# Kernel tuning notes

Measured on AMD Instinct MI355X. Metric: run time of the kernel, lower is better.

The kernel has to match this reference:

```python
import jax, jax.numpy as jnp
import numpy as np

B, S, D = 2, 4096, 768
H, W = 12, 128          # W = one-sided attention window; S % (2*W) == 0
DFF = 3072
HD = D // H
EPS = 1e-6


def band_attention(q, k, v, w):
    """Sliding-window (banded) attention, sliding_chunks-equivalent.
    q,k,v: (B, S, H, HD); q pre-scaled by 1/sqrt(HD).
    Returns context (B, S, D) and band probs (B, H, S, 2w+1)."""
    b, s, h, hd = q.shape
    n = s // w                                    # number of query blocks
    qb = q.reshape(b, n, w, h, hd)
    kp = jnp.pad(k, ((0, 0), (w, w), (0, 0), (0, 0)))   # zero-pad seq by w each side
    vp = jnp.pad(v, ((0, 0), (w, w), (0, 0), (0, 0)))
    # block i needs padded keys [i*w, i*w + 3w)  (blocks i-1, i, i+1)
    gidx = jnp.arange(n)[:, None] * w + jnp.arange(3 * w)[None, :]   # (n, 3w)
    kb = kp[:, gidx]                              # (b, n, 3w, h, hd)
    vb = vp[:, gidx]
    scores = jnp.einsum('bnthd,bnjhd->bhntj', qb, kb)   # (b,h,n,w,3w)
    t = jnp.arange(w)[:, None]                    # (w,1) pos within block
    j = jnp.arange(3 * w)[None, :]                # (1,3w)
    rel = j - w - t                               # relative key offset, valid in [-w,w]
    pos = jnp.arange(n)[:, None, None] * w + (j - w)     # (n,1,3w) global key pos
    valid = (jnp.abs(rel) <= w)[None] & (pos >= 0) & (pos < s)  # (n,w,3w)
    scores = jnp.where(valid[None, None], scores, -jnp.inf)
    probs = jax.nn.softmax(scores, axis=-1)
    out = jnp.einsum('bhntj,bnjhd->bnthd', probs, vb).reshape(b, s, h * hd)
    # extract the (2w+1) diagonals: offset d -> column j = t + d
    jj = jnp.arange(w)[:, None] + jnp.arange(2 * w + 1)[None, :]     # (w, 2w+1)
    attw = jnp.take_along_axis(probs, jj[None, None, None], axis=-1)
    return out, attw.reshape(b, h, s, 2 * w + 1)


def setup_inputs() -> dict:
    key = jax.random.key(0)
    ks = jax.random.split(key, 12)
    def lin(k, fan_in, shape):
        return (jax.random.normal(k, shape, jnp.float32) / np.sqrt(fan_in)).astype(jnp.float32)
    return {
        'src': jax.random.normal(ks[0], (B, S, D), jnp.float32),
        'Wq': lin(ks[1], D, (D, D)), 'bq': jnp.zeros((D,), jnp.float32),
        'Wk': lin(ks[2], D, (D, D)), 'bk': jnp.zeros((D,), jnp.float32),
        'Wv': lin(ks[3], D, (D, D)), 'bv': jnp.zeros((D,), jnp.float32),
        'W1': lin(ks[4], D, (D, DFF)), 'b1': jnp.zeros((DFF,), jnp.float32),
        'W2': lin(ks[5], DFF, (DFF, D)), 'b2': jnp.zeros((D,), jnp.float32),
        'g2': 1.0 + 0.1 * jax.random.normal(ks[6], (D,), jnp.float32),
        'beta2': 0.1 * jax.random.normal(ks[7], (D,), jnp.float32),
    }


def reference(src, Wq, bq, Wk, bk, Wv, bv, W1, b1, W2, b2, g2, beta2):
    b, s, d = src.shape
    # self-attention (allenai LongformerSelfAttention: q/k/v linears, no out proj)
    q = ((src @ Wq + bq) / np.sqrt(HD).astype(np.float32)).reshape(b, s, H, HD)
    k = (src @ Wk + bk).reshape(b, s, H, HD)
    v = (src @ Wv + bv).reshape(b, s, H, HD)
    attn_out, attn_w = band_attention(q, k, v, W)
    x = src + attn_out                      # residual (dropout=0, eval)
    # PositionalwiseFeedForward: Linear -> ReLU -> Linear
    ffn = jnp.maximum(x @ W1 + b1, 0.0) @ W2 + b2
    y = x + ffn
    # post-norm (normalize_before=False: only norm2 is applied)
    mu = jnp.mean(y, axis=-1, keepdims=True)
    var = jnp.mean(jnp.square(y - mu), axis=-1, keepdims=True)
    out = g2 * (y - mu) / jnp.sqrt(var + EPS) + beta2
    return out, attn_w
```

## Files before the change

kernel.cpp:

```cpp
#include <hip/hip_runtime.h>
#include <hip/hip_bf16.h>
#include <stdint.h>

#define NB 2
#define NS 4096
#define ND 768
#define NH 12
#define NW 128
#define NDFF 3072
#define NHD 64
#define NCH 32

typedef __attribute__((ext_vector_type(8))) short bf16x8;
typedef __attribute__((ext_vector_type(4))) short s16x4;
typedef __attribute__((ext_vector_type(4))) float f32x4;
typedef __attribute__((ext_vector_type(4))) int i32x4;

__device__ __forceinline__ float bf2f(short u) {
    union { unsigned int i; float f; } c;
    c.i = ((unsigned int)(unsigned short)u) << 16;
    return c.f;
}
__device__ __forceinline__ short f2bf(float f) {
    union { float f; unsigned int i; } c;
    c.f = f;
    unsigned int x = c.i;
    return (short)((x + 0x7fffu + ((x >> 16) & 1u)) >> 16);
}
__device__ __forceinline__ unsigned int cvtpk(float lo, float hi) {
    unsigned int r;
    asm("v_cvt_pk_bf16_f32 %0, %1, %2" : "=v"(r) : "v"(lo), "v"(hi));
    return r;
}
__device__ __forceinline__ float ubits_lo(unsigned u) {
    union { unsigned i; float f; } c; c.i = u << 16; return c.f;
}
__device__ __forceinline__ float ubits_hi(unsigned u) {
    union { unsigned i; float f; } c; c.i = u & 0xffff0000u; return c.f;
}

__device__ __forceinline__ void gl16(const void* g, const void* l) {
    __builtin_amdgcn_global_load_lds(
        (const __attribute__((address_space(1))) void*)g,
        (__attribute__((address_space(3))) void*)l, 16, 0, 0);
}

__global__ __launch_bounds__(256) void cast_bf16(const float* __restrict__ in,
                                                 short* __restrict__ out, int n4) {
    int i = blockIdx.x * 256 + threadIdx.x;
    if (i < n4) {
        f32x4 v = ((const f32x4*)in)[i];
        s16x4 o;
        o[0] = f2bf(v[0]); o[1] = f2bf(v[1]); o[2] = f2bf(v[2]); o[3] = f2bf(v[3]);
        ((s16x4*)out)[i] = o;
    }
}

__global__ __launch_bounds__(256) void transpose_cast(const float* __restrict__ in,
                                                      short* __restrict__ out,
                                                      int K, int N) {
    __shared__ float tile[32][33];
    int kb = blockIdx.y * 32, nb = blockIdx.x * 32;
    int tx = threadIdx.x & 31, ty = threadIdx.x >> 5;
    #pragma unroll
    for (int r = ty; r < 32; r += 8)
        tile[r][tx] = in[(long)(kb + r) * N + nb + tx];
    __syncthreads();
    #pragma unroll
    for (int r = ty; r < 32; r += 8)
        out[(long)(nb + r) * K + kb + tx] = f2bf(tile[tx][r]);
}

template<int MODE>
__global__ __launch_bounds__(256, 2) void gemmdb(
    const short* __restrict__ A,
    const short* __restrict__ Bt,
    const float* __restrict__ b0,
    const float* __restrict__ b1,
    const float* __restrict__ b2,
    void* __restrict__ outp,
    const short* __restrict__ xres,
    int M, int N, int K, int gx)
{
    __shared__ short lds[2][256 * 64];
    const int KT = K >> 6;

    int cpx = gridDim.x >> 3;
    int bid = blockIdx.x;
    int tile = (bid & 7) * cpx + (bid >> 3);
    int n0 = (tile % gx) * 128;
    int m0 = (tile / gx) * 128;

    int tid = threadIdx.x;
    int wid = tid >> 6, lane = tid & 63;
    int wr = wid >> 1, wc = wid & 1;
    int g = lane >> 4, lr = lane & 15;

    int rl = lane >> 3, sl = lane & 7;
    int soff = (sl ^ rl) << 3;
    const short* gA[4];
    const short* gB[4];
    #pragma unroll
    for (int c = 0; c < 4; ++c) {
        int row = c * 32 + wid * 8 + rl;
        gA[c] = A + (long)(m0 + row) * K + soff;
        gB[c] = Bt + (long)(n0 + row) * K + soff;
    }

    f32x4 acc[4][4];
    #pragma unroll
    for (int a = 0; a < 4; ++a)
        #pragma unroll
        for (int c = 0; c < 4; ++c)
            acc[a][c] = (f32x4){0.f, 0.f, 0.f, 0.f};

    auto stage = [&](int t, int buf) {
        long ko = (long)t << 6;
        #pragma unroll
        for (int c = 0; c < 4; ++c) {
            int lbase = (c * 32 + wid * 8) * 64;
            gl16(gA[c] + ko, &lds[buf][lbase]);
            gl16(gB[c] + ko, &lds[buf][128 * 64 + lbase]);
        }
    };

    stage(0, 0);
    asm volatile("s_waitcnt vmcnt(0)" ::: "memory");
    __builtin_amdgcn_s_barrier();

    int buf = 0;
    for (int t = 0; t < KT; ++t) {
        if (t + 1 < KT) stage(t + 1, buf ^ 1);
        const short* bufA = lds[buf];
        const short* bufB = lds[buf] + 128 * 64;
        bf16x8 af[2][4], bfr[2][4];
        #pragma unroll
        for (int kk = 0; kk < 2; ++kk) {
            int ph = (((kk << 2) + g) ^ (lr & 7)) << 3;
            #pragma unroll
            for (int mt = 0; mt < 4; ++mt)
                af[kk][mt] = *(const bf16x8*)&bufA[(wr * 64 + mt * 16 + lr) * 64 + ph];
            #pragma unroll
            for (int nt = 0; nt < 4; ++nt)
                bfr[kk][nt] = *(const bf16x8*)&bufB[(wc * 64 + nt * 16 + lr) * 64 + ph];
        }
        #pragma unroll
        for (int kk = 0; kk < 2; ++kk)
            #pragma unroll
            for (int mt = 0; mt < 4; ++mt)
                #pragma unroll
                for (int nt = 0; nt < 4; ++nt)
                    acc[mt][nt] = __builtin_amdgcn_mfma_f32_16x16x32_bf16(
                        af[kk][mt], bfr[kk][nt], acc[mt][nt], 0, 0, 0);
        asm volatile("s_waitcnt vmcnt(0)" ::: "memory");
        __builtin_amdgcn_s_barrier();
        buf ^= 1;
    }

    int mr0 = m0 + wr * 64;
    int nc0 = n0 + wc * 64;
    if (MODE == 4) {
        int proj = n0 / 768;
        const float* bp = (proj == 0) ? b0 : (proj == 1) ? b1 : b2;
        float scl = (proj == 0) ? 0.125f : 1.0f;
        short* obase = (short*)outp + (long)proj * ((long)NB * NS * ND);
        #pragma unroll
        for (int mt = 0; mt < 4; ++mt) {
            #pragma unroll
            for (int nt = 0; nt < 4; ++nt) {
                int c = nc0 + nt * 16 + lr - proj * 768;
                int hh = c >> 6, hd = c & 63;
                float bv = bp[c];
                if (proj == 2) {
                    int m = mr0 + mt * 16 + (g << 2);
                    int bbi = m >> 12, s = m & (NS - 1);
                    s16x4 ov;
                    ov[0] = f2bf(acc[mt][nt][0] + bv);
                    ov[1] = f2bf(acc[mt][nt][1] + bv);
                    ov[2] = f2bf(acc[mt][nt][2] + bv);
                    ov[3] = f2bf(acc[mt][nt][3] + bv);
                    *(s16x4*)&obase[((long)(bbi * NH + hh) * NHD + hd) * NS + s] = ov;
                } else {
                    #pragma unroll
                    for (int i = 0; i < 4; ++i) {
                        int m = mr0 + mt * 16 + (g << 2) + i;
                        int bbi = m >> 12, s = m & (NS - 1);
                        obase[((long)(bbi * NH + hh) * NS + s) * NHD + hd] =
                            f2bf((acc[mt][nt][i] + bv) * scl);
                    }
                }
            }
        }
    } else {
        #pragma unroll
        for (int mt = 0; mt < 4; ++mt) {
            #pragma unroll
            for (int nt = 0; nt < 4; ++nt) {
                int col = nc0 + nt * 16 + lr;
                float bv = b0[col];
                #pragma unroll
                for (int i = 0; i < 4; ++i) {
                    int m = mr0 + mt * 16 + (g << 2) + i;
                    float v = acc[mt][nt][i];
                    if (MODE == 2) {
                        v = fmaxf(v + bv, 0.f);
                        ((short*)outp)[(long)m * NDFF + col] = f2bf(v);
                    } else {
                        v = v + bv + bf2f(xres[(long)m * ND + col]);
                        ((float*)outp)[(long)m * ND + col] = v;
                    }
                }
            }
        }
    }
}

__global__ __launch_bounds__(512, 2) void attn_kernel(
    const short* __restrict__ qg,
    const short* __restrict__ kg,
    const short* __restrict__ vtg,
    const float* __restrict__ src,
    float* __restrict__ attw,
    short* __restrict__ xb)
{
    __shared__ short kvs[384 * 64];

    int blk = blockIdx.x;
    int ch = blk & 31;
    int tmp = blk >> 5;
    int h = tmp % NH;
    int b = tmp / NH;
    int tid = threadIdx.x;
    int wid = tid >> 6;
    int lane = tid & 63;
    int g = lane >> 4, lr = lane & 15;
    long bh = (long)(b * NH + h);
    long kbase = bh * NS * NHD;
    int srow0 = ch * NW;
    int t0 = wid << 4;
    int tl = t0 + lr;

    {
        int rsub = lane >> 3;
        int pc = lane & 7;
        int lc = pc ^ rsub;
        #pragma unroll
        for (int i = 0; i < 6; ++i) {
            int inst = wid * 6 + i;
            int j = inst * 8 + rsub;
            int s = srow0 - NW + j;
            s = s < 0 ? 0 : (s >= NS ? NS - 1 : s);
            gl16(&kg[kbase + (long)s * NHD + lc * 8], &kvs[inst * 512 + lane * 8]);
        }
    }
    bf16x8 aq[2];
    #pragma unroll
    for (int kk = 0; kk < 2; ++kk)
        aq[kk] = *(const bf16x8*)&qg[kbase + (long)(srow0 + tl) * NHD + (kk << 5) + (g << 3)];

    asm volatile("s_waitcnt vmcnt(0)" ::: "memory");
    __builtin_amdgcn_s_barrier();
    __builtin_amdgcn_sched_barrier(0);

    unsigned pku0[12][2], pku1[12][2];
    float m0, s0, m1, s1;
    auto half_pass = [&](int jtb, unsigned (&pk)[12][2], float& mh, float& sh) {
        f32x4 sc[12];
        #pragma unroll
        for (int q = 0; q < 12; ++q) {
            int jt = jtb + q;
            f32x4 a = (f32x4){0.f, 0.f, 0.f, 0.f};
            #pragma unroll
            for (int kk = 0; kk < 2; ++kk) {
                int phys = (((kk << 2) + g) ^ (lr & 7)) << 3;
                bf16x8 bk = *(const bf16x8*)&kvs[(jt * 16 + lr) * 64 + phys];
                a = __builtin_amdgcn_mfma_f32_16x16x32_bf16(bk, aq[kk], a, 0, 0, 0);
            }
            sc[q] = a;
        }
        float mx = -3.0e30f;
        #pragma unroll
        for (int q = 0; q < 12; ++q) {
            int j0 = (jtb + q) * 16 + (g << 2);
            #pragma unroll
            for (int i = 0; i < 4; ++i) {
                int j = j0 + i;
                int sp = srow0 - NW + j;
                bool ok = (sp >= 0) && (sp < NS) && (j >= tl) && (j <= tl + 2 * NW);
                float v = ok ? sc[q][i] : -3.0e30f;
                sc[q][i] = v;
                mx = fmaxf(mx, v);
            }
        }
        mx = fmaxf(mx, __shfl_xor(mx, 16, 64));
        mx = fmaxf(mx, __shfl_xor(mx, 32, 64));
        float sm = 0.f;
        #pragma unroll
        for (int q = 0; q < 12; ++q) {
            #pragma unroll
            for (int i = 0; i < 4; ++i) {
                float v = sc[q][i];
                float p = (v > -1.0e30f) ? __expf(v - mx) : 0.0f;
                sc[q][i] = p;
                sm += p;
            }
            pk[q][0] = cvtpk(sc[q][0], sc[q][1]);
            pk[q][1] = cvtpk(sc[q][2], sc[q][3]);
        }
        sm += __shfl_xor(sm, 16, 64);
        sm += __shfl_xor(sm, 32, 64);
        mh = mx; sh = sm;
    };

    auto stageV = [&](int hf) {
        #pragma unroll
        for (int i = 0; i < 3; ++i) {
            int v = wid * 3 + i;
            int fc = hf * 1536 + v * 64 + lane;
            int hd = fc / 48;
            int pc = fc % 48;
            int lc = (pc & ~7) | ((pc & 7) ^ (hd & 7));
            int scol = srow0 - NW + lc * 8;
            scol = scol < 0 ? 0 : (scol > NS - 8 ? NS - 8 : scol);
            gl16(&vtg[(bh * NHD + hd) * NS + scol],
                 &kvs[hf * 12288 + v * 512 + lane * 8]);
        }
    };

    half_pass(0, pku0, m0, s0);
    asm volatile("s_waitcnt lgkmcnt(0)" ::: "memory");
    __builtin_amdgcn_s_barrier();
    __builtin_amdgcn_sched_barrier(0);
    stageV(0);

    half_pass(12, pku1, m1, s1);
    asm volatile("s_waitcnt lgkmcnt(0)" ::: "memory");
    __builtin_amdgcn_s_barrier();
    __builtin_amdgcn_sched_barrier(0);
    stageV(1);

    float m = fmaxf(m0, m1);
    float r0 = __expf(m0 - m), r1 = __expf(m1 - m);
    float inv = 1.0f / (s0 * r0 + s1 * r1);
    float w0 = r0 * inv, w1 = r1 * inv;
    #pragma unroll
    for (int q = 0; q < 12; ++q) {
        #pragma unroll
        for (int u = 0; u < 2; ++u) {
            pku0[q][u] = cvtpk(ubits_lo(pku0[q][u]) * w0, ubits_hi(pku0[q][u]) * w0);
            pku1[q][u] = cvtpk(ubits_lo(pku1[q][u]) * w1, ubits_hi(pku1[q][u]) * w1);
        }
    }

    asm volatile("s_waitcnt vmcnt(0)" ::: "memory");
    __builtin_amdgcn_s_barrier();
    __builtin_amdgcn_sched_barrier(0);

    int lA = ((g & 1) << 5) + lr;
    int lB = lA + 16;
    bool hi_ = (g & 2) != 0;
    long awrow = (bh * NS + srow0 + tl) * 257;
    f32x4 o[4];
    #pragma unroll
    for (int nt = 0; nt < 4; ++nt) o[nt] = (f32x4){0.f, 0.f, 0.f, 0.f};

    #pragma unroll
    for (int kt = 0; kt < 12; ++kt) {
        const unsigned* pa = (kt < 6) ? pku0[2 * kt]     : pku1[2 * kt - 12];
        const unsigned* pb = (kt < 6) ? pku0[2 * kt + 1] : pku1[2 * kt - 11];
        int a0 = __shfl((int)pa[0], lA, 64);
        int a1 = __shfl((int)pa[1], lA, 64);
        int a2 = __shfl((int)pa[0], lB, 64);
        int a3 = __shfl((int)pa[1], lB, 64);
        int b0 = __shfl((int)pb[0], lA, 64);
        int b1 = __shfl((int)pb[1], lA, 64);
        int b2 = __shfl((int)pb[0], lB, 64);
        int b3 = __shfl((int)pb[1], lB, 64);
        i32x4 wi;
        wi[0] = hi_ ? b0 : a0;
        wi[1] = hi_ ? b1 : a1;
        wi[2] = hi_ ? b2 : a2;
        wi[3] = hi_ ? b3 : a3;
        bf16x8 af = *(bf16x8*)&wi;

        {
            float pv_[8];
            #pragma unroll
            for (int p = 0; p < 4; ++p) {
                unsigned u = (unsigned)wi[p];
                pv_[2 * p]     = ubits_lo(u);
                pv_[2 * p + 1] = ubits_hi(u);
            }
            int c0 = kt * 32 + (g << 3) - tl;
            if (c0 >= 0 && c0 <= 2 * NW - 7) {
                f32x4 v0 = {pv_[0], pv_[1], pv_[2], pv_[3]};
                f32x4 v1 = {pv_[4], pv_[5], pv_[6], pv_[7]};
                *(f32x4*)&attw[awrow + c0] = v0;
                *(f32x4*)&attw[awrow + c0 + 4] = v1;
            } else {
                #pragma unroll
                for (int e = 0; e < 8; ++e) {
                    int c = c0 + e;
                    if (c >= 0 && c <= 2 * NW)
                        attw[awrow + c] = pv_[e];
                }
            }
        }

        #pragma unroll
        for (int nt = 0; nt < 4; ++nt) {
            int c = kt * 4 + g;
            int phys = ((c & ~7) | ((c & 7) ^ (lr & 7))) << 3;
            bf16x8 bv = *(const bf16x8*)&kvs[(nt * 16 + lr) * 384 + phys];
            o[nt] = __builtin_amdgcn_mfma_f32_16x16x32_bf16(af, bv, o[nt], 0, 0, 0);
        }
    }

    #pragma unroll
    for (int nt = 0; nt < 4; ++nt) {
        int d = nt * 16 + lr;
        int dcol = h * NHD + d;
        #pragma unroll
        for (int i = 0; i < 4; ++i) {
            int t = t0 + (g << 2) + i;
            long row = (long)b * NS + srow0 + t;
            float v = o[nt][i] + src[row * ND + dcol];
            xb[row * ND + dcol] = f2bf(v);
        }
    }
}

__global__ __launch_bounds__(256) void ln_kernel(float* __restrict__ y,
                                                 const float* __restrict__ g2,
                                                 const float* __restrict__ beta2) {
    int row = blockIdx.x;
    long base = (long)row * ND;
    int tid = threadIdx.x;
    float v[3];
    float s = 0.f, ss = 0.f;
    #pragma unroll
    for (int i = 0; i < 3; ++i) {
        v[i] = y[base + i * 256 + tid];
        s += v[i];
        ss += v[i] * v[i];
    }
    #pragma unroll
    for (int m = 1; m < 64; m <<= 1) {
        s += __shfl_xor(s, m, 64);
        ss += __shfl_xor(ss, m, 64);
    }
    __shared__ float red[8];
    int wid = tid >> 6, lane = tid & 63;
    if (lane == 0) { red[wid] = s; red[wid + 4] = ss; }
    __syncthreads();
    s = red[0] + red[1] + red[2] + red[3];
    ss = red[4] + red[5] + red[6] + red[7];
    float mu = s * (1.0f / ND);
    float var = ss * (1.0f / ND) - mu * mu;
    float rstd = rsqrtf(var + 1e-6f);
    #pragma unroll
    for (int i = 0; i < 3; ++i) {
        int c = i * 256 + tid;
        y[base + c] = g2[c] * (v[i] - mu) * rstd + beta2[c];
    }
}

extern "C" void kernel_launch(void* const* d_in, const int* in_sizes, int n_in,
                              void* d_out, int out_size, void* d_ws, size_t ws_size,
                              hipStream_t stream) {
    const float* src  = (const float*)d_in[0];
    const float* Wq   = (const float*)d_in[1];
    const float* bq   = (const float*)d_in[2];
    const float* Wk   = (const float*)d_in[3];
    const float* bk   = (const float*)d_in[4];
    const float* Wv   = (const float*)d_in[5];
    const float* bv   = (const float*)d_in[6];
    const float* W1   = (const float*)d_in[7];
    const float* b1   = (const float*)d_in[8];
    const float* W2   = (const float*)d_in[9];
    const float* b2   = (const float*)d_in[10];
    const float* g2   = (const float*)d_in[11];
    const float* bt2  = (const float*)d_in[12];

    float* out  = (float*)d_out;
    float* attw = out + (long)NB * NS * ND;

    char* ws = (char*)d_ws;
    const size_t SZ_XF  = (size_t)NB * NS * ND * 4;
    const size_t SZ_XB  = (size_t)NB * NS * ND * 2;
    const size_t SZ_W1T = (size_t)ND * NDFF * 2;
    const size_t SZ_W2T = (size_t)NDFF * ND * 2;
    const size_t SZ_QKV = (size_t)NB * NS * ND * 2;
    const size_t SZ_WT  = (size_t)ND * ND * 2;

    short* x_bf  = (short*)(ws + SZ_XF);
    short* W1T   = (short*)(ws + SZ_XF + SZ_XB);
    short* W2T   = (short*)(ws + SZ_XF + SZ_XB + SZ_W1T);
    char*  regA  = ws + SZ_XF + SZ_XB + SZ_W1T + SZ_W2T;
    short* srcb  = (short*)regA;
    short* WqT   = (short*)(regA + SZ_QKV);
    short* qb    = (short*)(regA + SZ_QKV + 3 * SZ_WT);
    short* kb_   = (short*)(regA + 2 * SZ_QKV + 3 * SZ_WT);
    short* vb_   = (short*)(regA + 3 * SZ_QKV + 3 * SZ_WT);
    short* WkT   = WqT + (size_t)768 * ND;
    short* WvT   = WqT + (size_t)1536 * ND;
    short* hbuf  = (short*)regA;

    const int M = NB * NS;

    cast_bf16<<<(M * ND / 4 + 255) / 256, 256, 0, stream>>>(src, srcb, M * ND / 4);
    transpose_cast<<<dim3(ND / 32, ND / 32), 256, 0, stream>>>(Wq, WqT, ND, ND);
    transpose_cast<<<dim3(ND / 32, ND / 32), 256, 0, stream>>>(Wk, WkT, ND, ND);
    transpose_cast<<<dim3(ND / 32, ND / 32), 256, 0, stream>>>(Wv, WvT, ND, ND);
    transpose_cast<<<dim3(NDFF / 32, ND / 32), 256, 0, stream>>>(W1, W1T, ND, NDFF);
    transpose_cast<<<dim3(ND / 32, NDFF / 32), 256, 0, stream>>>(W2, W2T, NDFF, ND);

    gemmdb<4><<<(2304 / 128) * (M / 128), 256, 0, stream>>>(
        srcb, WqT, bq, bk, bv, qb, nullptr, M, 2304, ND, 2304 / 128);

    attn_kernel<<<NB * NH * NCH, 512, 0, stream>>>(qb, kb_, vb_, src, attw, x_bf);

    gemmdb<2><<<(NDFF / 128) * (M / 128), 256, 0, stream>>>(
        x_bf, W1T, b1, b1, b1, hbuf, nullptr, M, NDFF, ND, NDFF / 128);
    gemmdb<3><<<(ND / 128) * (M / 128), 256, 0, stream>>>(
        hbuf, W2T, b2, b2, b2, out, x_bf, M, ND, NDFF, ND / 128);

    ln_kernel<<<M, 256, 0, stream>>>(out, g2, bt2);
}
```

Measured before the change: 231.3 us.

## Add 256x256 eight-wave GEMM with 8-phase pipelining for QKV and FFN1

Introduces a new GEMM kernel with 256x256 output tiles, 512 threads and 128KB of dynamic LDS. It splits each K-tile into eight phases that interleave global-to-LDS prefetch with MFMA, using barriers and s_setprio. The QKV projection and the first FFN linear use this kernel, and the W2 GEMM keeps the old 128x128 kernel. Larger tiles increase data reuse per tile, but they also mean far fewer blocks (e.g. 288 for QKV) and lower occupancy, so the GPU may be less well filled.

```diff
diff --git a/kernel.cpp b/kernel.cpp
--- a/kernel.cpp
+++ b/kernel.cpp
@@ -71,101 +71,121 @@
         out[(long)(nb + r) * K + kb + tx] = f2bf(tile[tx][r]);
 }
 
+#define GPH(BUF, MB, KK, STMT, WT)                                            \
+    {                                                                          \
+        const char* db = smem + (BUF) * 65536;                                 \
+        if ((MB) == 0) {                                                       \
+            bfr[0] = *(const bf16x8*)(db + boff + 0 * 2048 + pk##KK);          \
+            bfr[1] = *(const bf16x8*)(db + boff + 1 * 2048 + pk##KK);          \
+            bfr[2] = *(const bf16x8*)(db + boff + 2 * 2048 + pk##KK);          \
+            bfr[3] = *(const bf16x8*)(db + boff + 3 * 2048 + pk##KK);          \
+        }                                                                      \
+        af[0] = *(const bf16x8*)(db + aoff + ((MB) + 0) * 2048 + pk##KK);      \
+        af[1] = *(const bf16x8*)(db + aoff + ((MB) + 1) * 2048 + pk##KK);      \
+        af[2] = *(const bf16x8*)(db + aoff + ((MB) + 2) * 2048 + pk##KK);      \
+        af[3] = *(const bf16x8*)(db + aoff + ((MB) + 3) * 2048 + pk##KK);      \
+        STMT;                                                                  \
+        __builtin_amdgcn_s_barrier();                                          \
+        asm volatile("s_waitcnt lgkmcnt(0)" ::: "memory");                     \
+        __builtin_amdgcn_s_setprio(1);                                         \
+        _Pragma("unroll")                                                      \
+        for (int mm = 0; mm < 4; ++mm)                                         \
+            _Pragma("unroll")                                                  \
+            for (int nn = 0; nn < 4; ++nn)                                     \
+                acc[(MB) + mm][nn] = __builtin_amdgcn_mfma_f32_16x16x32_bf16(  \
+                    af[mm], bfr[nn], acc[(MB) + mm][nn], 0, 0, 0);             \
+        __builtin_amdgcn_s_setprio(0);                                         \
+        WT;                                                                    \
+        __builtin_amdgcn_s_barrier();                                          \
+    }
+
 template<int MODE>
-__global__ __launch_bounds__(256, 2) void gemmdb(
+__global__ __launch_bounds__(512, 2) void gemm8p(
     const short* __restrict__ A,
     const short* __restrict__ Bt,
     const float* __restrict__ b0,
     const float* __restrict__ b1,
     const float* __restrict__ b2,
     void* __restrict__ outp,
-    const short* __restrict__ xres,
     int M, int N, int K, int gx)
 {
-    __shared__ short lds[2][256 * 64];
+    extern __shared__ char smem[];
     const int KT = K >> 6;
-
     int cpx = gridDim.x >> 3;
     int bid = blockIdx.x;
     int tile = (bid & 7) * cpx + (bid >> 3);
-    int n0 = (tile % gx) * 128;
-    int m0 = (tile / gx) * 128;
-
+    int n0 = (tile % gx) * 256;
+    int m0 = (tile / gx) * 256;
     int tid = threadIdx.x;
     int wid = tid >> 6, lane = tid & 63;
-    int wr = wid >> 1, wc = wid & 1;
+    int wm = wid >> 2, wn = wid & 3;
     int g = lane >> 4, lr = lane & 15;
 
-    int rl = lane >> 3, sl = lane & 7;
-    int soff = (sl ^ rl) << 3;
-    const short* gA[4];
-    const short* gB[4];
-    #pragma unroll
-    for (int c = 0; c < 4; ++c) {
-        int row = c * 32 + wid * 8 + rl;
-        gA[c] = A + (long)(m0 + row) * K + soff;
-        gB[c] = Bt + (long)(n0 + row) * K + soff;
-    }
-
-    f32x4 acc[4][4];
-    #pragma unroll
-    for (int a = 0; a < 4; ++a)
+    int r0s = tid >> 3;
+    int lc0 = (tid & 7) ^ (r0s & 7);
+    int r1s = r0s + 64;
+    int lc1 = (tid & 7) ^ (r1s & 7);
+    const short* pA0 = A + (long)(m0 + r0s) * K + lc0 * 8;
+    const short* pA1 = A + (long)(m0 + r1s) * K + lc1 * 8;
+    const short* pB0 = Bt + (long)(n0 + r0s) * K + lc0 * 8;
+    const short* pB1 = Bt + (long)(n0 + r1s) * K + lc1 * 8;
+    const long hstep = (long)128 * K;
+
+    f32x4 acc[8][4];
+    #pragma unroll
+    for (int a = 0; a < 8; ++a)
         #pragma unroll
         for (int c = 0; c < 4; ++c)
             acc[a][c] = (f32x4){0.f, 0.f, 0.f, 0.f};
-
-    auto stage = [&](int t, int buf) {
-        long ko = (long)t << 6;
-        #pragma unroll
-        for (int c = 0; c < 4; ++c) {
-            int lbase = (c * 32 + wid * 8) * 64;
-            gl16(gA[c] + ko, &lds[buf][lbase]);
-            gl16(gB[c] + ko, &lds[buf][128 * 64 + lbase]);
+    bf16x8 af[4], bfr[4];
+
+    int aoff = wm * 16384 + lr * 128;
+    int boff = 32768 + (wn >> 1) * 16384 + ((wn & 1) * 64 + lr) * 128;
+    int pk0 = (g ^ (lr & 7)) << 4;
+    int pk1 = ((4 + g) ^ (lr & 7)) << 4;
+
+    auto stg = [&](int kt, int isB, int half) {
+        char* l = smem + (kt & 1) * 65536 + isB * 32768 + half * 16384 + tid * 16;
+        long off = (long)half * hstep + ((long)kt << 6);
+        if (isB) {
+            gl16(pB0 + off, l);
+            gl16(pB1 + off, l + 8192);
+        } else {
+            gl16(pA0 + off, l);
+            gl16(pA1 + off, l + 8192);
         }
     };
 
-    stage(0, 0);
-    asm volatile("s_waitcnt vmcnt(0)" ::: "memory");
+    stg(0, 1, 0); stg(0, 1, 1); stg(0, 0, 0); stg(0, 0, 1);
+    stg(1, 1, 0);
+    asm volatile("s_waitcnt vmcnt(2)" ::: "memory");
     __builtin_amdgcn_s_barrier();
 
-    int buf = 0;
-    for (int t = 0; t < KT; ++t) {
-        if (t + 1 < KT) stage(t + 1, buf ^ 1);
-        const short* bufA = lds[buf];
-        const short* bufB = lds[buf] + 128 * 64;
-        bf16x8 af[2][4], bfr[2][4];
-        #pragma unroll
-        for (int kk = 0; kk < 2; ++kk) {
-            int ph = (((kk << 2) + g) ^ (lr & 7)) << 3;
-            #pragma unroll
-            for (int mt = 0; mt < 4; ++mt)
-                af[kk][mt] = *(const bf16x8*)&bufA[(wr * 64 + mt * 16 + lr) * 64 + ph];
-            #pragma unroll
-            for (int nt = 0; nt < 4; ++nt)
-                bfr[kk][nt] = *(const bf16x8*)&bufB[(wc * 64 + nt * 16 + lr) * 64 + ph];
-        }
-        #pragma unroll
-        for (int kk = 0; kk < 2; ++kk)
-            #pragma unroll
-            for (int mt = 0; mt < 4; ++mt)
-                #pragma unroll
-                for (int nt = 0; nt < 4; ++nt)
-                    acc[mt][nt] = __builtin_amdgcn_mfma_f32_16x16x32_bf16(
-                        af[kk][mt], bfr[kk][nt], acc[mt][nt], 0, 0, 0);
-        asm volatile("s_waitcnt vmcnt(0)" ::: "memory");
-        __builtin_amdgcn_s_barrier();
-        buf ^= 1;
-    }
-
-    int mr0 = m0 + wr * 64;
-    int nc0 = n0 + wc * 64;
+    for (int it = 0, t = 0; it < (KT >> 1); ++it, t += 2) {
+        bool s2 = (t + 2) < KT, s3 = (t + 3) < KT;
+        GPH(0, 0, 0, stg(t + 1, 1, 1), ;)
+        GPH(0, 4, 0, stg(t + 1, 0, 0), ;)
+        GPH(0, 0, 1, stg(t + 1, 0, 1), ;)
+        GPH(0, 4, 1, if (s2) stg(t + 2, 1, 0),
+            if (s2) { asm volatile("s_waitcnt vmcnt(2)" ::: "memory"); }
+            else    { asm volatile("s_waitcnt vmcnt(0)" ::: "memory"); })
+        GPH(1, 0, 0, if (s2) stg(t + 2, 1, 1), ;)
+        GPH(1, 4, 0, if (s2) stg(t + 2, 0, 0), ;)
+        GPH(1, 0, 1, if (s2) stg(t + 2, 0, 1), ;)
+        GPH(1, 4, 1, if (s3) stg(t + 3, 1, 0),
+            if (s3) { asm volatile("s_waitcnt vmcnt(2)" ::: "memory"); }
+            else    { asm volatile("s_waitcnt vmcnt(0)" ::: "memory"); })
+    }
+
+    int mr0 = m0 + wm * 128;
+    int nc0 = n0 + wn * 64;
     if (MODE == 4) {
         int proj = n0 / 768;
         const float* bp = (proj == 0) ? b0 : (proj == 1) ? b1 : b2;
         float scl = (proj == 0) ? 0.125f : 1.0f;
         short* obase = (short*)outp + (long)proj * ((long)NB * NS * ND);
         #pragma unroll
-        for (int mt = 0; mt < 4; ++mt) {
+        for (int mt = 0; mt < 8; ++mt) {
             #pragma unroll
             for (int nt = 0; nt < 4; ++nt) {
                 int c = nc0 + nt * 16 + lr - proj * 768;
@@ -193,7 +213,7 @@
         }
     } else {
         #pragma unroll
-        for (int mt = 0; mt < 4; ++mt) {
+        for (int mt = 0; mt < 8; ++mt) {
             #pragma unroll
             for (int nt = 0; nt < 4; ++nt) {
                 int col = nc0 + nt * 16 + lr;
@@ -201,15 +221,111 @@
                 #pragma unroll
                 for (int i = 0; i < 4; ++i) {
                     int m = mr0 + mt * 16 + (g << 2) + i;
-                    float v = acc[mt][nt][i];
-                    if (MODE == 2) {
-                        v = fmaxf(v + bv, 0.f);
-                        ((short*)outp)[(long)m * NDFF + col] = f2bf(v);
-                    } else {
-                        v = v + bv + bf2f(xres[(long)m * ND + col]);
-                        ((float*)outp)[(long)m * ND + col] = v;
-                    }
+                    float v = fmaxf(acc[mt][nt][i] + bv, 0.f);
+                    ((short*)outp)[(long)m * NDFF + col] = f2bf(v);
                 }
+            }
+        }
+    }
+}
+
+template<int MODE>
+__global__ __launch_bounds__(256, 2) void gemmdb(
+    const short* __restrict__ A,
+    const short* __restrict__ Bt,
+    const float* __restrict__ b0,
+    void* __restrict__ outp,
+    const short* __restrict__ xres,
+    int M, int N, int K, int gx)
+{
+    __shared__ short lds[2][256 * 64];
+    const int KT = K >> 6;
+
+    int cpx = gridDim.x >> 3;
+    int bid = blockIdx.x;
+    int tile = (bid & 7) * cpx + (bid >> 3);
+    int n0 = (tile % gx) * 128;
+    int m0 = (tile / gx) * 128;
+
+    int tid = threadIdx.x;
+    int wid = tid >> 6, lane = tid & 63;
+    int wr = wid >> 1, wc = wid & 1;
+    int g = lane >> 4, lr = lane & 15;
+
+    int rl = lane >> 3, sl = lane & 7;
+    int soff = (sl ^ rl) << 3;
+    const short* gA[4];
+    const short* gB[4];
+    #pragma unroll
+    for (int c = 0; c < 4; ++c) {
+        int row = c * 32 + wid * 8 + rl;
+        gA[c] = A + (long)(m0 + row) * K + soff;
+        gB[c] = Bt + (long)(n0 + row) * K + soff;
+    }
+
+    f32x4 acc[4][4];
+    #pragma unroll
+    for (int a = 0; a < 4; ++a)
+        #pragma unroll
+        for (int c = 0; c < 4; ++c)
+            acc[a][c] = (f32x4){0.f, 0.f, 0.f, 0.f};
+
+    auto stage = [&](int t, int buf) {
+        long ko = (long)t << 6;
+        #pragma unroll
+        for (int c = 0; c < 4; ++c) {
+            int lbase = (c * 32 + wid * 8) * 64;
+            gl16(gA[c] + ko, &lds[buf][lbase]);
+            gl16(gB[c] + ko, &lds[buf][128 * 64 + lbase]);
+        }
+    };
+
+    stage(0, 0);
+    asm volatile("s_waitcnt vmcnt(0)" ::: "memory");
+    __builtin_amdgcn_s_barrier();
+
+    int buf = 0;
+    for (int t = 0; t < KT; ++t) {
+        if (t + 1 < KT) stage(t + 1, buf ^ 1);
+        const short* bufA = lds[buf];
+        const short* bufB = lds[buf] + 128 * 64;
+        bf16x8 af[2][4], bfr[2][4];
+        #pragma unroll
+        for (int kk = 0; kk < 2; ++kk) {
+            int ph = (((kk << 2) + g) ^ (lr & 7)) << 3;
+            #pragma unroll
+            for (int mt = 0; mt < 4; ++mt)
+                af[kk][mt] = *(const bf16x8*)&bufA[(wr * 64 + mt * 16 + lr) * 64 + ph];
+            #pragma unroll
+            for (int nt = 0; nt < 4; ++nt)
+                bfr[kk][nt] = *(const bf16x8*)&bufB[(wc * 64 + nt * 16 + lr) * 64 + ph];
+        }
+        #pragma unroll
+        for (int kk = 0; kk < 2; ++kk)
+            #pragma unroll
+            for (int mt = 0; mt < 4; ++mt)
+                #pragma unroll
+                for (int nt = 0; nt < 4; ++nt)
+                    acc[mt][nt] = __builtin_amdgcn_mfma_f32_16x16x32_bf16(
+                        af[kk][mt], bfr[kk][nt], acc[mt][nt], 0, 0, 0);
+        asm volatile("s_waitcnt vmcnt(0)" ::: "memory");
+        __builtin_amdgcn_s_barrier();
+        buf ^= 1;
+    }
+
+    int mr0 = m0 + wr * 64;
+    int nc0 = n0 + wc * 64;
+    #pragma unroll
+    for (int mt = 0; mt < 4; ++mt) {
+        #pragma unroll
+        for (int nt = 0; nt < 4; ++nt) {
+            int col = nc0 + nt * 16 + lr;
+            float bv = b0[col];
+            #pragma unroll
+            for (int i = 0; i < 4; ++i) {
+                int m = mr0 + mt * 16 + (g << 2) + i;
+                float v = acc[mt][nt][i] + bv + bf2f(xres[(long)m * ND + col]);
+                ((float*)outp)[(long)m * ND + col] = v;
             }
         }
     }
@@ -515,15 +631,20 @@
     transpose_cast<<<dim3(NDFF / 32, ND / 32), 256, 0, stream>>>(W1, W1T, ND, NDFF);
     transpose_cast<<<dim3(ND / 32, NDFF / 32), 256, 0, stream>>>(W2, W2T, NDFF, ND);
 
-    gemmdb<4><<<(2304 / 128) * (M / 128), 256, 0, stream>>>(
-        srcb, WqT, bq, bk, bv, qb, nullptr, M, 2304, ND, 2304 / 128);
+    (void)hipFuncSetAttribute(reinterpret_cast<const void*>(gemm8p<4>),
+                              hipFuncAttributeMaxDynamicSharedMemorySize, 131072);
+    (void)hipFuncSetAttribute(reinterpret_cast<const void*>(gemm8p<2>),
+                              hipFuncAttributeMaxDynamicSharedMemorySize, 131072);
+
+    gemm8p<4><<<(2304 / 256) * (M / 256), 512, 131072, stream>>>(
+        srcb, WqT, bq, bk, bv, qb, M, 2304, ND, 2304 / 256);
 
     attn_kernel<<<NB * NH * NCH, 512, 0, stream>>>(qb, kb_, vb_, src, attw, x_bf);
 
-    gemmdb<2><<<(NDFF / 128) * (M / 128), 256, 0, stream>>>(
-        x_bf, W1T, b1, b1, b1, hbuf, nullptr, M, NDFF, ND, NDFF / 128);
+    gemm8p<2><<<(NDFF / 256) * (M / 256), 512, 131072, stream>>>(
+        x_bf, W1T, b1, b1, b1, hbuf, M, NDFF, ND, NDFF / 256);
     gemmdb<3><<<(ND / 128) * (M / 128), 256, 0, stream>>>(
-        hbuf, W2T, b2, b2, b2, out, x_bf, M, ND, NDFF, ND / 128);
+        hbuf, W2T, b2, out, x_bf, M, ND, NDFF, ND / 128);
 
     ln_kernel<<<M, 256, 0, stream>>>(out, g2, bt2);
 }
```

Measured after the change: 242.4 us. 1.05x slower.

## Merge weight transposes and input cast into one prep kernel; remap attention blocks

Applied to the files above, without the earlier changes.

Folds the six separate prep launches (src cast plus five weight transpose-casts) into a single kernel that picks its job from the block index, removing launch overhead and the small-grid tail gaps between them. The attention kernel also permutes its block index so consecutive block ids spread across the 8 XCDs in a different interleave, which changes locality of K/V reuse. Adds branching per block and relies on hardcoded block counts matching the shapes.

```diff
diff --git a/kernel.cpp b/kernel.cpp
--- a/kernel.cpp
+++ b/kernel.cpp
@@ -45,22 +45,37 @@
         (__attribute__((address_space(3))) void*)l, 16, 0, 0);
 }
 
-__global__ __launch_bounds__(256) void cast_bf16(const float* __restrict__ in,
-                                                 short* __restrict__ out, int n4) {
-    int i = blockIdx.x * 256 + threadIdx.x;
-    if (i < n4) {
-        f32x4 v = ((const f32x4*)in)[i];
+__global__ __launch_bounds__(256) void prep_kernel(
+    const float* __restrict__ Wq, const float* __restrict__ Wk,
+    const float* __restrict__ Wv, const float* __restrict__ W1,
+    const float* __restrict__ W2, const float* __restrict__ src,
+    short* __restrict__ WqkvT, short* __restrict__ W1T,
+    short* __restrict__ W2T,   short* __restrict__ srcb)
+{
+    int id = blockIdx.x;
+    if (id >= 6336) {
+        int i = (id - 6336) * 256 + threadIdx.x;
+        f32x4 v = ((const f32x4*)src)[i];
         s16x4 o;
         o[0] = f2bf(v[0]); o[1] = f2bf(v[1]); o[2] = f2bf(v[2]); o[3] = f2bf(v[3]);
-        ((s16x4*)out)[i] = o;
-    }
-}
-
-__global__ __launch_bounds__(256) void transpose_cast(const float* __restrict__ in,
-                                                      short* __restrict__ out,
-                                                      int K, int N) {
+        ((s16x4*)srcb)[i] = o;
+        return;
+    }
     __shared__ float tile[32][33];
-    int kb = blockIdx.y * 32, nb = blockIdx.x * 32;
+    const float* in; short* out; int K, N, bx, by;
+    if (id < 1728) {
+        int z = id / 576, t = id % 576;
+        in = (z == 0) ? Wq : (z == 1) ? Wk : Wv;
+        out = WqkvT + (size_t)z * ND * ND;
+        K = ND; N = ND; bx = t % 24; by = t / 24;
+    } else if (id < 4032) {
+        int t = id - 1728;
+        in = W1; out = W1T; K = ND; N = NDFF; bx = t % 96; by = t / 96;
+    } else {
+        int t = id - 4032;
+        in = W2; out = W2T; K = NDFF; N = ND; bx = t % 24; by = t / 24;
+    }
+    int kb = by * 32, nb = bx * 32;
     int tx = threadIdx.x & 31, ty = threadIdx.x >> 5;
     #pragma unroll
     for (int r = ty; r < 32; r += 8)
@@ -225,7 +240,8 @@
 {
     __shared__ short kvs[384 * 64];
 
-    int blk = blockIdx.x;
+    int bid = blockIdx.x;
+    int blk = (bid & 7) * (NB * NH * NCH / 8) + (bid >> 3);
     int ch = blk & 31;
     int tmp = blk >> 5;
     int h = tmp % NH;
@@ -502,18 +518,12 @@
     short* qb    = (short*)(regA + SZ_QKV + 3 * SZ_WT);
     short* kb_   = (short*)(regA + 2 * SZ_QKV + 3 * SZ_WT);
     short* vb_   = (short*)(regA + 3 * SZ_QKV + 3 * SZ_WT);
-    short* WkT   = WqT + (size_t)768 * ND;
-    short* WvT   = WqT + (size_t)1536 * ND;
     short* hbuf  = (short*)regA;
 
     const int M = NB * NS;
 
-    cast_bf16<<<(M * ND / 4 + 255) / 256, 256, 0, stream>>>(src, srcb, M * ND / 4);
-    transpose_cast<<<dim3(ND / 32, ND / 32), 256, 0, stream>>>(Wq, WqT, ND, ND);
-    transpose_cast<<<dim3(ND / 32, ND / 32), 256, 0, stream>>>(Wk, WkT, ND, ND);
-    transpose_cast<<<dim3(ND / 32, ND / 32), 256, 0, stream>>>(Wv, WvT, ND, ND);
-    transpose_cast<<<dim3(NDFF / 32, ND / 32), 256, 0, stream>>>(W1, W1T, ND, NDFF);
-    transpose_cast<<<dim3(ND / 32, NDFF / 32), 256, 0, stream>>>(W2, W2T, NDFF, ND);
+    prep_kernel<<<12480, 256, 0, stream>>>(Wq, Wk, Wv, W1, W2, src,
+                                           WqT, W1T, W2T, srcb);
 
     gemmdb<4><<<(2304 / 128) * (M / 128), 256, 0, stream>>>(
         srcb, WqT, bq, bk, bv, qb, nullptr, M, 2304, ND, 2304 / 128);
```

New measurement: 216.9 us. 1.07x faster.
